# Kernel optimization log

Measured on AMD Instinct MI355X. Metric: run time of the kernel, lower is better.

The kernel has to match this reference:

```python
import math
import numpy as np
import jax
import jax.numpy as jnp
from jax import lax

B, N, F, C, L = 256, 256, 512, 512, 3
RATIO, NEG, BIG_NEG = 0.8, 0.2, -1e9


def setup_inputs():
    key = jax.random.key(0)
    ks = jax.random.split(key, 16)
    g = lambda k, shape, s=0.05: (jax.random.normal(k, shape) * s).astype(jnp.float32)
    x_ids = jax.random.randint(ks[0], (B, N), 0, F)
    graph_prompt_ids = jax.random.randint(ks[1], (B,), 0, F)
    u = jax.random.uniform(ks[2], (B, N, N))
    adj = (u < 16.0 / N).astype(jnp.float32)
    adj = jnp.maximum(adj, jnp.swapaxes(adj, 1, 2))  # undirected
    return dict(
        x_ids=x_ids, graph_prompt_ids=graph_prompt_ids, adj=adj,
        emb=g(ks[3], (F, F), 0.02),
        conv_W=g(ks[4], (L, C, C)), conv_b=jnp.zeros((L, C), jnp.float32),
        att_src=g(ks[5], (L, C)), att_dst=g(ks[6], (L, C)),
        q_W=g(ks[7], (L, C, C)), q_b=jnp.zeros((L, C), jnp.float32),
        att_w=g(ks[8], (L, 2 * C)), att_b=jnp.zeros((L,), jnp.float32),
        gcn_W=g(ks[9], (L, C, C)), gcn_b=jnp.zeros((L, C), jnp.float32),
        le_W1=g(ks[10], (L, C)), le_b1=jnp.zeros((L,), jnp.float32),
        le_W2=g(ks[11], (L, C)), le_W3=g(ks[12], (L, C)),
        lin1_W=g(ks[13], (2 * C, C)), lin1_b=jnp.zeros((C,), jnp.float32),
        lin2_W=g(ks[14], (C, F - 1)), lin2_b=jnp.zeros((F - 1,), jnp.float32),
    )


def _gat(x, mask, W, b, a_src, a_dst):
    # GATConv (heads=1): alpha_ij = softmax_j leaky_relu(a_dst.h_i + a_src.h_j)
    h = x @ W                                   # [B,n,C]
    si = h @ a_dst                              # [B,n] dst term
    sj = h @ a_src                              # [B,n] src term
    logit = jnp.where(mask, jax.nn.leaky_relu(si[:, :, None] + sj[:, None, :], NEG), BIG_NEG)
    att = jax.nn.softmax(logit, axis=-1)
    return jnp.einsum('bij,bjc->bic', att, h) + b


def _gcn(x, A, W, b):
    deg = A.sum(-1)
    d = jnp.where(deg > 0, lax.rsqrt(deg), 0.0)
    return jnp.einsum('bij,bjc->bic', A * d[:, :, None] * d[:, None, :], x @ W) + b


def _neighbor_max(xp, mask):
    # Xq[b,i,c] = max_{j: mask[b,i,j]} xp[b,j,c]; scan over j avoids a [B,n,n,C] tensor
    def step(carry, inp):
        xpj, mj = inp                            # [B,C], [B,n]
        return jnp.maximum(carry, jnp.where(mj[:, :, None], xpj[:, None, :], BIG_NEG)), None
    init = jnp.full(xp.shape, BIG_NEG, xp.dtype)
    Xq, _ = lax.scan(step, init, (jnp.swapaxes(xp, 0, 1), jnp.transpose(mask, (2, 0, 1))))
    return Xq


def _asap_pool(x, A, mask, k, qW, qb, aw, ab, gW, gb, w1, b1, w2, w3):
    c = x.shape[-1]
    xp = _gcn(x, A, gW, gb)                      # intra-cluster GCN
    Xq = _neighbor_max(xp, mask)                 # master query per cluster
    Mq = Xq @ qW + qb
    si = Mq @ aw[:c]
    sj = xp @ aw[c:]
    logit = jnp.where(mask, jax.nn.leaky_relu(si[:, :, None] + sj[:, None, :] + ab, NEG), BIG_NEG)
    S = jax.nn.softmax(logit, axis=-1)           # soft cluster assignment [B,n,n]
    xc = jnp.einsum('bij,bjc->bic', S, x)        # cluster representations
    # LEConv fitness: lin1(x_i) + sum_j A_ij (lin2(x_i) - lin3(x_j)), output dim 1
    deg = A.sum(-1)
    fit = jax.nn.sigmoid(xc @ w1 + b1 + (xc @ w2) * deg - jnp.einsum('bij,bj->bi', A, xc @ w3))
    vals, perm = lax.top_k(fit, k)               # per-graph top-k clusters (static k)
    xk = jnp.take_along_axis(xc, perm[:, :, None], axis=1) * vals[:, :, None]
    Sk = jnp.take_along_axis(S, perm[:, :, None], axis=1)    # [B,k,n]
    SA = jnp.einsum('bkn,bnm->bkm', Sk, A)
    A_new = jnp.einsum('bkm,blm->bkl', SA, Sk)   # S A S^T coarsened adjacency
    diag = jnp.diagonal(A_new, axis1=1, axis2=2)
    A_new = A_new + jnp.eye(k, dtype=A_new.dtype) * jnp.where(diag <= 0, 1.0, 0.0)[:, :, None]
    return xk, A_new, A_new > 0


def _forward(x_ids, adj, emb, conv_W, conv_b, att_src, att_dst, q_W, q_b, att_w, att_b,
             gcn_W, gcn_b, le_W1, le_b1, le_W2, le_W3, lin1_W, lin1_b, lin2_W, lin2_b):
    A = jnp.maximum(adj, jnp.eye(N, dtype=adj.dtype))        # add self loops, weight 1
    mask = A > 0
    x = emb[x_ids]                                           # [B,N,F] embedding lookup
    n, xs = N, None
    for l in range(L):
        k = int(math.ceil(RATIO * n))
        x = jax.nn.relu(_gat(x, mask, conv_W[l], conv_b[l], att_src[l], att_dst[l]))
        x, A, mask = _asap_pool(x, A, mask, k, q_W[l], q_b[l], att_w[l], att_b[l],
                                gcn_W[l], gcn_b[l], le_W1[l], le_b1[l], le_W2[l], le_W3[l])
        r = jnp.concatenate([x.mean(axis=1), x.max(axis=1)], axis=-1)  # scatter mean/max readout
        xs = r if xs is None else xs + r
        n = k
    h = jax.nn.relu(xs @ lin1_W + lin1_b)
    return h @ lin2_W + lin2_b                               # [B, F-1]


def reference(x_ids, graph_prompt_ids, adj, emb, conv_W, conv_b, att_src, att_dst,
              q_W, q_b, att_w, att_b, gcn_W, gcn_b, le_W1, le_b1, le_W2, le_W3,
              lin1_W, lin1_b, lin2_W, lin2_b):
    del graph_prompt_ids  # unused in the original forward body
    return _forward(x_ids, adj, emb, conv_W, conv_b, att_src, att_dst, q_W, q_b,
                    att_w, att_b, gcn_W, gcn_b, le_W1, le_b1, le_W2, le_W3,
                    lin1_W, lin1_b, lin2_W, lin2_b)
```

## Files before the change

kernel.cpp:

```cpp
#include <hip/hip_runtime.h>
#include <math.h>

#define NB   256
#define NMAX 256
#define CH   512
#define LD2  256
#define LDC  512
#define BS2  (256*256)
#define BSC  (256*512)

typedef _Float16 f16;
typedef __attribute__((ext_vector_type(4))) f16 f16x4;
typedef __attribute__((ext_vector_type(8))) f16 f16x8;
typedef __attribute__((ext_vector_type(4))) float f32x4;

#define INV2048 4.8828125e-04f

__device__ __forceinline__ float warp_sum_f(float v) {
#pragma unroll
  for (int m = 32; m >= 1; m >>= 1) v += __shfl_xor(v, m);
  return v;
}

__device__ __forceinline__ void split1(float x, f16& h, f16& l) {
  float xh = (__builtin_fabsf(x) >= 6.103515625e-05f) ? x : 0.f;
  f16 hh = (f16)xh;
  float hf = (float)hh;
  h = hh;
  l = (f16)((x - hf) * 2048.0f);
}

__device__ __forceinline__ float rc(f16 h, f16 l) {
  return (float)h + (float)l * INV2048;
}

__device__ __forceinline__ float rc8q(const f16x8& h, const f16x8& l, int q) {
  return (float)h[q] + (float)l[q] * INV2048;
}

template <int BMODE>
__global__ __launch_bounds__(256, 2)
void pgemm_kernel(const f16* __restrict__ Ahp, const f16* __restrict__ Alp, long bsA, int lda,
                  const f16* __restrict__ Bhp, const f16* __restrict__ Blp, long bsB, int ldb,
                  f16* __restrict__ Yh, f16* __restrict__ Yl, float* __restrict__ Yf,
                  long bsY, int ldy,
                  const float* __restrict__ bias, const float* __restrict__ rowscale,
                  int M, int Ncol, int K, int flags)
{
  __shared__ f16 Ah[64][40];
  __shared__ f16 Al[64][40];
  __shared__ f16 Bh[128][40];
  __shared__ f16 Bl[128][40];

  const int gx = gridDim.x, gy = gridDim.y;
  const int nwg = gx * gy * gridDim.z;
  const int lin = blockIdx.x + gx * (blockIdx.y + gy * blockIdx.z);
  const int q8 = nwg >> 3, r8 = nwg & 7;
  const int xcd = lin & 7, sub = lin >> 3;
  const int swz = ((xcd < r8) ? xcd * (q8 + 1) : r8 * (q8 + 1) + (xcd - r8) * q8) + sub;
  const int bxi = swz % gx;
  const int tmp = swz / gx;
  const int byi = tmp % gy;
  const int b   = tmp / gy;

  const int i0  = byi * 64;
  const int n0  = bxi * 128;
  const int tid = threadIdx.x;
  const int w  = tid >> 6, l = tid & 63;
  const int wr = (w >> 1) * 32, wc = (w & 1) * 64;
  const int lr = l & 15, lq = l >> 4;
  const f16* Abh = Ahp + (long)b * bsA;
  const f16* Abl = Alp + (long)b * bsA;
  const f16* Bbh = Bhp + (long)b * bsB;
  const f16* Bbl = Blp + (long)b * bsB;

  f32x4 acc1[2][4], acc2[2][4];
#pragma unroll
  for (int mi = 0; mi < 2; ++mi)
#pragma unroll
    for (int ni = 0; ni < 4; ++ni) {
      acc1[mi][ni] = (f32x4){0.f, 0.f, 0.f, 0.f};
      acc2[mi][ni] = (f32x4){0.f, 0.f, 0.f, 0.f};
    }

  const f16x8 z8 = (f16x8){0,0,0,0,0,0,0,0};
  f16x8 rah, ral;
  f16x8 rbh[2], rbl[2];
  f16x8 rva, rvb, rwa, rwb;

  const int arow = tid >> 2, akq = (tid & 3) * 8;

  auto LOADA = [&](int k0) {
    int gr = i0 + arow, gk = k0 + akq;
    rah = z8; ral = z8;
    if (gr < M) {
      if (gk + 7 < K) {
        rah = *(const f16x8*)(Abh + (long)gr * lda + gk);
        ral = *(const f16x8*)(Abl + (long)gr * lda + gk);
      } else {
#pragma unroll
        for (int j = 0; j < 8; ++j) if (gk + j < K) {
          rah[j] = Abh[(long)gr * lda + gk + j];
          ral[j] = Abl[(long)gr * lda + gk + j];
        }
      }
    }
  };
  auto STOREA = [&]() {
    *(f16x8*)&Ah[arow][akq] = rah;
    *(f16x8*)&Al[arow][akq] = ral;
  };
  auto LOADB = [&](int k0) {
    if (BMODE == 0) {
#pragma unroll
      for (int rep = 0; rep < 2; ++rep) {
        int idx = rep * 256 + tid;
        int c = idx >> 2, kq = (idx & 3) * 8;
        int gc = n0 + c, gk = k0 + kq;
        rbh[rep] = z8; rbl[rep] = z8;
        if (gc < Ncol) {
          if (gk + 7 < K) {
            rbh[rep] = *(const f16x8*)(Bbh + (long)gc * ldb + gk);
            rbl[rep] = *(const f16x8*)(Bbl + (long)gc * ldb + gk);
          } else {
#pragma unroll
            for (int j = 0; j < 8; ++j) if (gk + j < K) {
              rbh[rep][j] = Bbh[(long)gc * ldb + gk + j];
              rbl[rep][j] = Bbl[(long)gc * ldb + gk + j];
            }
          }
        }
      }
    } else {
      int c8  = (tid >> 4) * 8;
      int k0p = (tid & 15) * 2;
      int gc = n0 + c8;
      rva = z8; rvb = z8; rwa = z8; rwb = z8;
      int gka = k0 + k0p, gkb = gka + 1;
      if (gc + 7 < Ncol) {
        if (gka < K) { rva = *(const f16x8*)(Bbh + (long)gka * ldb + gc);
                       rwa = *(const f16x8*)(Bbl + (long)gka * ldb + gc); }
        if (gkb < K) { rvb = *(const f16x8*)(Bbh + (long)gkb * ldb + gc);
                       rwb = *(const f16x8*)(Bbl + (long)gkb * ldb + gc); }
      }
    }
  };
  auto STOREB = [&]() {
    if (BMODE == 0) {
#pragma unroll
      for (int rep = 0; rep < 2; ++rep) {
        int idx = rep * 256 + tid;
        int c = idx >> 2, kq = (idx & 3) * 8;
        *(f16x8*)&Bh[c][kq] = rbh[rep];
        *(f16x8*)&Bl[c][kq] = rbl[rep];
      }
    } else {
      int c8  = (tid >> 4) * 8;
      int k0p = (tid & 15) * 2;
#pragma unroll
      for (int j = 0; j < 8; ++j) {
        union { f16 f[2]; unsigned u; } ph, pl;
        ph.f[0] = rva[j]; ph.f[1] = rvb[j];
        pl.f[0] = rwa[j]; pl.f[1] = rwb[j];
        *(unsigned*)&Bh[c8 + j][k0p] = ph.u;
        *(unsigned*)&Bl[c8 + j][k0p] = pl.u;
      }
    }
  };

  const int nk = (K + 31) / 32;
  LOADA(0); LOADB(0);
  for (int ki = 0; ki < nk; ++ki) {
    STOREA(); STOREB();
    __syncthreads();
    if (ki + 1 < nk) { LOADA((ki + 1) * 32); LOADB((ki + 1) * 32); }

    f16x8 bh[4], bl[4];
#pragma unroll
    for (int ni = 0; ni < 4; ++ni) {
      bh[ni] = *(const f16x8*)&Bh[wc + ni * 16 + lr][lq * 8];
      bl[ni] = *(const f16x8*)&Bl[wc + ni * 16 + lr][lq * 8];
    }
#pragma unroll
    for (int mi = 0; mi < 2; ++mi) {
      f16x8 ah = *(const f16x8*)&Ah[wr + mi * 16 + lr][lq * 8];
      f16x8 al = *(const f16x8*)&Al[wr + mi * 16 + lr][lq * 8];
#pragma unroll
      for (int ni = 0; ni < 4; ++ni) {
        acc1[mi][ni] = __builtin_amdgcn_mfma_f32_16x16x32_f16(ah, bh[ni], acc1[mi][ni], 0, 0, 0);
        acc2[mi][ni] = __builtin_amdgcn_mfma_f32_16x16x32_f16(ah, bl[ni], acc2[mi][ni], 0, 0, 0);
        acc2[mi][ni] = __builtin_amdgcn_mfma_f32_16x16x32_f16(al, bh[ni], acc2[mi][ni], 0, 0, 0);
      }
    }
    __syncthreads();
  }

#pragma unroll
  for (int mi = 0; mi < 2; ++mi) {
#pragma unroll
    for (int ni = 0; ni < 4; ++ni) {
      int col = n0 + wc + ni * 16 + lr;
      if (col >= Ncol) continue;
      float bv = (flags & 1) ? bias[col] : 0.f;
#pragma unroll
      for (int r = 0; r < 4; ++r) {
        int row = i0 + wr + mi * 16 + lq * 4 + r;
        if (row >= M) continue;
        float vv = acc1[mi][ni][r] + acc2[mi][ni][r] * INV2048;
        if (flags & 4) vv *= rowscale[b * 256 + row];
        vv += bv;
        if (flags & 2) vv = fmaxf(vv, 0.f);
        long off = (long)b * bsY + (long)row * ldy + col;
        if (flags & 8) { f16 h, lo; split1(vv, h, lo); Yh[off] = h; Yl[off] = lo; }
        if (flags & 16) Yf[off] = vv;
      }
    }
  }
}

__global__ void presplit_kernel(const float* __restrict__ W, f16* __restrict__ Wh,
                                f16* __restrict__ Wl, int K, int N) {
  int n = blockIdx.x;
  for (int k = threadIdx.x; k < K; k += blockDim.x) {
    f16 h, l; split1(W[(long)k * N + n], h, l);
    Wh[(long)n * K + k] = h;
    Wl[(long)n * K + k] = l;
  }
}

__global__ void splitbuf_kernel(const float* __restrict__ X, f16* __restrict__ Xh,
                                f16* __restrict__ Xl, int cols) {
  int i = blockIdx.x;
  for (int c = threadIdx.x; c < cols; c += blockDim.x) {
    f16 h, l; split1(X[(long)i * cols + c], h, l);
    Xh[(long)i * cols + c] = h;
    Xl[(long)i * cols + c] = l;
  }
}

__global__ void build_a_deg_kernel(const float* __restrict__ adj, f16* __restrict__ AAh,
                                   f16* __restrict__ AAl, float* __restrict__ deg,
                                   float* __restrict__ dinv) {
  int b = blockIdx.y, i = blockIdx.x, j = threadIdx.x;
  __shared__ float red[256];
  float v = adj[(long)b * BS2 + i * 256 + j];
  if (i == j) v = fmaxf(v, 1.f);
  f16 h, l; split1(v, h, l);
  long o = (long)b * BS2 + i * 256 + j;
  AAh[o] = h; AAl[o] = l;
  red[j] = v; __syncthreads();
  for (int s = 128; s > 0; s >>= 1) { if (j < s) red[j] += red[j + s]; __syncthreads(); }
  if (j == 0) {
    float s = red[0];
    deg[b * 256 + i] = s;
    dinv[b * 256 + i] = (s > 0.f) ? (1.f / sqrtf(s)) : 0.f;
  }
}

__global__ void embed_kernel(const int* __restrict__ ids, const float* __restrict__ emb,
                             f16* __restrict__ Xh, f16* __restrict__ Xl) {
  int b = blockIdx.y, i = blockIdx.x, t = threadIdx.x;
  int id = ids[b * NMAX + i];
  float4 v = *(const float4*)(emb + (long)id * CH + t * 4);
  long o = (long)b * BSC + (long)i * LDC + t * 4;
  float vv[4] = {v.x, v.y, v.z, v.w};
#pragma unroll
  for (int j = 0; j < 4; ++j) { f16 h, l; split1(vv[j], h, l); Xh[o + j] = h; Xl[o + j] = l; }
}

__global__ void rowdot_kernel(const f16* __restrict__ Xh, const f16* __restrict__ Xl,
                              const float* __restrict__ v1, const float* __restrict__ v2,
                              const float* __restrict__ v3,
                              float* __restrict__ o1, float* __restrict__ o2,
                              float* __restrict__ o3, int nvec) {
  int b = blockIdx.y, i = blockIdx.x, lane = threadIdx.x;
  long base = (long)b * BSC + (long)i * LDC;
  float a1 = 0.f, a2 = 0.f, a3 = 0.f;
  for (int c = lane; c < CH; c += 64) {
    float x = rc(Xh[base + c], Xl[base + c]);
    a1 = fmaf(x, v1[c], a1);
    if (nvec > 1) a2 = fmaf(x, v2[c], a2);
    if (nvec > 2) a3 = fmaf(x, v3[c], a3);
  }
  a1 = warp_sum_f(a1);
  if (nvec > 1) a2 = warp_sum_f(a2);
  if (nvec > 2) a3 = warp_sum_f(a3);
  if (lane == 0) {
    o1[b * 256 + i] = a1;
    if (nvec > 1) o2[b * 256 + i] = a2;
    if (nvec > 2) o3[b * 256 + i] = a3;
  }
}

__global__ void vq_kernel(const float* __restrict__ qW, const float* __restrict__ qb,
                          const float* __restrict__ aw, float* __restrict__ v,
                          float* __restrict__ c0) {
  int blk = blockIdx.x, lane = threadIdx.x;
  if (blk < 512) {
    float s = 0.f;
    for (int j = lane; j < CH; j += 64) s = fmaf(qW[(long)blk * CH + j], aw[j], s);
    s = warp_sum_f(s);
    if (lane == 0) v[blk] = s;
  } else {
    float s = 0.f;
    for (int j = lane; j < CH; j += 64) s = fmaf(qb[j], aw[j], s);
    s = warp_sum_f(s);
    if (lane == 0) c0[0] = s;
  }
}

__global__ __launch_bounds__(256)
void softmax_kernel(const f16* __restrict__ AAh, const f16* __restrict__ AAl,
                    const float* __restrict__ si, const float* __restrict__ sj,
                    const float* __restrict__ attb,
                    f16* __restrict__ Ph, f16* __restrict__ Pl, int n, int masked) {
  int b = blockIdx.y, i = blockIdx.x, j = threadIdx.x;
  __shared__ float red[256];
  float logit = -1e30f, e = 0.f;
  float siv = si[b * 256 + i];
  long ro = (long)b * BS2 + i * 256;
  if (j < n) {
    float z = siv + sj[b * 256 + j] + (attb ? attb[0] : 0.f);
    z = (z > 0.f) ? z : 0.2f * z;
    if (masked) {
      float a = rc(AAh[ro + j], AAl[ro + j]);
      logit = (a > 0.f) ? z : -1e9f;
    } else logit = z;
  }
  red[j] = logit; __syncthreads();
  for (int s = 128; s > 0; s >>= 1) { if (j < s) red[j] = fmaxf(red[j], red[j + s]); __syncthreads(); }
  float mx = red[0]; __syncthreads();
  if (j < n) e = expf(logit - mx);
  red[j] = e; __syncthreads();
  for (int s = 128; s > 0; s >>= 1) { if (j < s) red[j] += red[j + s]; __syncthreads(); }
  float sum = red[0];
  if (j < n) {
    f16 h, l; split1(e / sum, h, l);
    Ph[ro + j] = h; Pl[ro + j] = l;
  }
}

__global__ __launch_bounds__(512)
void colmax_kernel(const f16* __restrict__ XPh, const f16* __restrict__ XPl,
                   const float* __restrict__ v, const float* __restrict__ c0,
                   float* __restrict__ si_full, int n) {
  int b = blockIdx.x, t = threadIdx.x;
  int cg = t >> 3, rl = t & 7, c0c = cg * 8;
  long base = (long)b * BSC;
  __shared__ float red[64];
  float m[8];
#pragma unroll
  for (int q = 0; q < 8; ++q) m[q] = -1e9f;
  for (int j = rl; j < n; j += 8) {
    f16x8 h = *(const f16x8*)(XPh + base + (long)j * LDC + c0c);
    f16x8 l = *(const f16x8*)(XPl + base + (long)j * LDC + c0c);
#pragma unroll
    for (int q = 0; q < 8; ++q) m[q] = fmaxf(m[q], rc8q(h, l, q));
  }
#pragma unroll
  for (int d = 1; d < 8; d <<= 1)
#pragma unroll
    for (int q = 0; q < 8; ++q) m[q] = fmaxf(m[q], __shfl_xor(m[q], d));
  if (rl == 0) {
    float p = 0.f;
#pragma unroll
    for (int q = 0; q < 8; ++q) p = fmaf(m[q], v[c0c + q], p);
    red[cg] = p;
  }
  __syncthreads();
  for (int s = 32; s > 0; s >>= 1) { if (t < s) red[t] += red[t + s]; __syncthreads(); }
  if (t == 0) si_full[b] = red[0] + c0[0];
}

__global__ __launch_bounds__(256)
void nbrdot_kernel(const f16* __restrict__ AAh, const f16* __restrict__ AAl,
                   const f16* __restrict__ XPh, const f16* __restrict__ XPl,
                   const float* __restrict__ v, const float* __restrict__ c0,
                   const float* __restrict__ si_full, float* __restrict__ si, int n) {
  int b = blockIdx.y, i = blockIdx.x, t = threadIdx.x;
  __shared__ int list[256];
  __shared__ int cnt, nmiss;
  __shared__ float red[256];
  if (t == 0) { cnt = 0; nmiss = 0; }
  __syncthreads();
  long ro = (long)b * BS2 + i * 256;
  if (t < n) {
    float a = rc(AAh[ro + t], AAl[ro + t]);
    if (a > 0.f) { int p = atomicAdd(&cnt, 1); list[p] = t; }
    else atomicAdd(&nmiss, 1);
  }
  __syncthreads();
  if (nmiss == 0) {
    if (t == 0) si[b * 256 + i] = si_full[b];
    return;
  }
  int c = cnt;
  long base = (long)b * BSC;
  float m1 = -1e9f, m2 = -1e9f;
  for (int q = 0; q < c; ++q) {
    int j = list[q];
    m1 = fmaxf(m1, rc(XPh[base + (long)j * LDC + t], XPl[base + (long)j * LDC + t]));
    m2 = fmaxf(m2, rc(XPh[base + (long)j * LDC + t + 256], XPl[base + (long)j * LDC + t + 256]));
  }
  red[t] = m1 * v[t] + m2 * v[t + 256];
  __syncthreads();
  for (int s = 128; s > 0; s >>= 1) { if (t < s) red[t] += red[t + s]; __syncthreads(); }
  if (t == 0) si[b * 256 + i] = red[0] + c0[0];
}

__global__ void fit_kernel(const f16* __restrict__ AAh, const f16* __restrict__ AAl,
                           const float* __restrict__ t1, const float* __restrict__ t2,
                           const float* __restrict__ t3,
                           const float* __restrict__ deg, const float* __restrict__ leb1,
                           float* __restrict__ fit, int n) {
  int b = blockIdx.y, i = blockIdx.x, lane = threadIdx.x;
  long ro = (long)b * BS2 + i * 256;
  float s = 0.f;
  for (int j = lane; j < n; j += 64) s = fmaf(rc(AAh[ro + j], AAl[ro + j]), t3[b * 256 + j], s);
  s = warp_sum_f(s);
  if (lane == 0) {
    float z = t1[b * 256 + i] + leb1[0] + t2[b * 256 + i] * deg[b * 256 + i] - s;
    fit[b * 256 + i] = 1.f / (1.f + expf(-z));
  }
}

__global__ __launch_bounds__(256)
void topk_kernel(const float* __restrict__ fit, int* __restrict__ perm,
                 float* __restrict__ vals, int n, int k) {
  __shared__ float v[256];
  __shared__ int ix[256];
  int b = blockIdx.x, t = threadIdx.x;
  v[t] = (t < n) ? fit[b * 256 + t] : -1e30f;
  ix[t] = t;
  __syncthreads();
  for (int size = 2; size <= 256; size <<= 1)
    for (int str = size >> 1; str > 0; str >>= 1) {
      int p = t ^ str;
      if (p > t) {
        bool desc = ((t & size) == 0);
        float v1 = v[t], v2 = v[p]; int i1 = ix[t], i2 = ix[p];
        bool inorder = (v1 > v2) || (v1 == v2 && i1 < i2);
        if (inorder != desc) { v[t] = v2; v[p] = v1; ix[t] = i2; ix[p] = i1; }
      }
      __syncthreads();
    }
  if (t < k) { perm[b * 256 + t] = ix[t]; vals[b * 256 + t] = v[t]; }
}

__global__ __launch_bounds__(256)
void gather_kernel(const f16* __restrict__ Hh, const f16* __restrict__ Hl,
                   const f16* __restrict__ Ph, const f16* __restrict__ Pl,
                   const int* __restrict__ perm, const float* __restrict__ vals,
                   f16* __restrict__ Xh, f16* __restrict__ Xl,
                   f16* __restrict__ Skh, f16* __restrict__ Skl, int n) {
  int b = blockIdx.y, p = blockIdx.x, t = threadIdx.x;
  int src = perm[b * 256 + p];
  float sv = vals[b * 256 + p];
#pragma unroll
  for (int r = 0; r < 2; ++r) {
    int c = t + r * 256;
    long so = (long)b * BSC + (long)src * LDC + c;
    long dof = (long)b * BSC + (long)p * LDC + c;
    float x = rc(Hh[so], Hl[so]) * sv;
    f16 h, l; split1(x, h, l);
    Xh[dof] = h; Xl[dof] = l;
  }
  if (t < n) {
    long so = (long)b * BS2 + src * 256 + t;
    long dof = (long)b * BSC + p * 256 + t;
    Skh[dof] = Ph[so]; Skl[dof] = Pl[so];
  }
}

__global__ void degfix_kernel(f16* __restrict__ AAh, f16* __restrict__ AAl,
                              float* __restrict__ deg, float* __restrict__ dinv, int k) {
  int b = blockIdx.y, i = blockIdx.x, j = threadIdx.x;
  __shared__ float red[256];
  long ro = (long)b * BS2 + i * 256;
  float v = 0.f;
  if (j < k) {
    v = rc(AAh[ro + j], AAl[ro + j]);
    if (j == i && v <= 0.f) {
      v += 1.f;
      f16 h, l; split1(v, h, l);
      AAh[ro + j] = h; AAl[ro + j] = l;
    }
  }
  red[j] = v; __syncthreads();
  for (int s = 128; s > 0; s >>= 1) { if (j < s) red[j] += red[j + s]; __syncthreads(); }
  if (j == 0) {
// ... 240 lines not shown
                  const float* __restrict__ w3, const float* __restrict__ leb1,
                  float* __restrict__ xs, int n) {
  int b = blockIdx.x, t = threadIdx.x;
  int cg = t >> 3, rl = t & 7, c0c = cg * 8;
  long baseC = (long)b * BSC;
  __shared__ float red[512];
  __shared__ float xc2[512];

  float s8[8];
#pragma unroll
  for (int q = 0; q < 8; ++q) s8[q] = 0.f;
  for (int j = rl; j < n; j += 8) {
    f16x8 h = *(const f16x8*)(Xh + baseC + (long)j * LDC + c0c);
    f16x8 l = *(const f16x8*)(Xl + baseC + (long)j * LDC + c0c);
#pragma unroll
    for (int q = 0; q < 8; ++q) s8[q] += rc8q(h, l, q);
  }
#pragma unroll
  for (int d = 1; d < 8; d <<= 1)
#pragma unroll
    for (int q = 0; q < 8; ++q) s8[q] += __shfl_xor(s8[q], d);
  float invn = 1.f / (float)n;
  if (rl == 0) {
#pragma unroll
    for (int q = 0; q < 8; ++q) xc2[c0c + q] = s8[q] * invn;
  }
  __syncthreads();

  float x2 = xc2[t];
  red[t] = x2 * w1[t]; __syncthreads();
  for (int s2 = 256; s2 > 0; s2 >>= 1) { if (t < s2) red[t] += red[t + s2]; __syncthreads(); }
  float a1 = red[0]; __syncthreads();
  red[t] = x2 * w2[t]; __syncthreads();
  for (int s2 = 256; s2 > 0; s2 >>= 1) { if (t < s2) red[t] += red[t + s2]; __syncthreads(); }
  float a2 = red[0]; __syncthreads();
  red[t] = x2 * w3[t]; __syncthreads();
  for (int s2 = 256; s2 > 0; s2 >>= 1) { if (t < s2) red[t] += red[t + s2]; __syncthreads(); }
  float a3 = red[0]; __syncthreads();

  float alpha = sc[b * 16 + 2], deg3 = sc[b * 16 + 3];
  float sub = 0.f;
  for (int j = 0; j < n; ++j) sub += alpha * a3;
  float z = a1 + leb1[0] + a2 * deg3 - sub;
  float fv = 1.f / (1.f + expf(-z));
  xs[b * 1024 + t] += fv * x2;
  xs[b * 1024 + 512 + t] += fv * x2;
  (void)Hh; (void)Hl; (void)gb;
}

extern "C" void kernel_launch(void* const* d_in, const int* in_sizes, int n_in,
                              void* d_out, int out_size, void* d_ws, size_t ws_size,
                              hipStream_t stream) {
  (void)in_sizes; (void)n_in; (void)out_size;
  const int*   x_ids  = (const int*)  d_in[0];
  const float* adj    = (const float*)d_in[2];
  const float* emb    = (const float*)d_in[3];
  const float* conv_W = (const float*)d_in[4];
  const float* conv_b = (const float*)d_in[5];
  const float* att_src= (const float*)d_in[6];
  const float* att_dst= (const float*)d_in[7];
  const float* q_W    = (const float*)d_in[8];
  const float* q_b    = (const float*)d_in[9];
  const float* att_w  = (const float*)d_in[10];
  const float* att_b  = (const float*)d_in[11];
  const float* gcn_W  = (const float*)d_in[12];
  const float* gcn_b  = (const float*)d_in[13];
  const float* le_W1  = (const float*)d_in[14];
  const float* le_b1  = (const float*)d_in[15];
  const float* le_W2  = (const float*)d_in[16];
  const float* le_W3  = (const float*)d_in[17];
  const float* lin1_W = (const float*)d_in[18];
  const float* lin1_b = (const float*)d_in[19];
  const float* lin2_W = (const float*)d_in[20];
  const float* lin2_b = (const float*)d_in[21];
  float* out = (float*)d_out;

  const size_t WN_CONV = 3u * CH * CH;
  const size_t WN_GCN  = 3u * CH * CH;
  const size_t WN_L1   = (size_t)(2 * CH) * CH;
  const size_t WN_L2   = (size_t)CH * 511;
  const size_t WTOT    = WN_CONV + WN_GCN + WN_L1 + WN_L2;

  const size_t per_b  = (size_t)(3 * BSC * 4 + 2 * BS2 * 4 + 11 * 256 * 4
                                 + (4 * 512 + 2 * 256 + 16) * 4 + 4096);
  const size_t fixedb = (size_t)(3 * 512 + 64 + NB * 1024 + NB * 512) * 4
                      + WTOT * 4 + (size_t)NB * 1024 * 4 + (size_t)NB * 512 * 4;
  const size_t slack  = 64 * 512;
  int bc = 4;
  for (int cand = 256; cand >= 4; cand >>= 1) {
    if ((size_t)cand * per_b + fixedb + slack <= ws_size) { bc = cand; break; }
  }
  const int nchunks = NB / bc;

  char* w = (char*)d_ws;
  auto alloc = [&](size_t bytes) { char* p = w; w += (bytes + 255) & ~(size_t)255; return p; };
  float* xs   = (float*)alloc(sizeof(float) * NB * 1024);
  float* vvec = (float*)alloc(sizeof(float) * 3 * CH);
  float* c0   = (float*)alloc(256);
  f16*   Wh   = (f16*)alloc(WTOT * 2);
  f16*   Wl   = (f16*)alloc(WTOT * 2);
  f16*   XSh  = (f16*)alloc((size_t)NB * 1024 * 2);
  f16*   XSl  = (f16*)alloc((size_t)NB * 1024 * 2);
  f16*   FHh  = (f16*)alloc((size_t)NB * 512 * 2);
  f16*   FHl  = (f16*)alloc((size_t)NB * 512 * 2);
  f16* Xh  = (f16*)alloc((size_t)bc * BSC * 2);
  f16* Xl  = (f16*)alloc((size_t)bc * BSC * 2);
  f16* Hh  = (f16*)alloc((size_t)bc * BSC * 2);
  f16* Hl  = (f16*)alloc((size_t)bc * BSC * 2);
  f16* XPh = (f16*)alloc((size_t)bc * BSC * 2);
  f16* XPl = (f16*)alloc((size_t)bc * BSC * 2);
  f16* Ph  = (f16*)alloc((size_t)bc * BS2 * 2);
  f16* Pl  = (f16*)alloc((size_t)bc * BS2 * 2);
  f16* AAh = (f16*)alloc((size_t)bc * BS2 * 2);
  f16* AAl = (f16*)alloc((size_t)bc * BS2 * 2);
  float* si   = (float*)alloc(sizeof(float) * bc * NMAX);
  float* sj   = (float*)alloc(sizeof(float) * bc * NMAX);
  float* deg  = (float*)alloc(sizeof(float) * bc * NMAX);
  float* dinv = (float*)alloc(sizeof(float) * bc * NMAX);
  float* t1   = (float*)alloc(sizeof(float) * bc * NMAX);
  float* t2   = (float*)alloc(sizeof(float) * bc * NMAX);
  float* t3   = (float*)alloc(sizeof(float) * bc * NMAX);
  float* fit  = (float*)alloc(sizeof(float) * bc * NMAX);
  float* vals = (float*)alloc(sizeof(float) * bc * NMAX);
  int*   perm = (int*)  alloc(sizeof(int)   * bc * NMAX);
  float* sifu = (float*)alloc(sizeof(float) * bc);
  float* wv   = (float*)alloc(sizeof(float) * bc * 256);
  float* xcr  = (float*)alloc(sizeof(float) * bc * 512);
  float* h3   = (float*)alloc(sizeof(float) * bc * 512);
  float* sc   = (float*)alloc(sizeof(float) * bc * 16);
  f16* xcrh   = (f16*)alloc((size_t)bc * 512 * 2);
  f16* xcrl   = (f16*)alloc((size_t)bc * 512 * 2);

  f16* cwh = Wh;                       f16* cwl = Wl;
  f16* gwh = Wh + WN_CONV;             f16* gwl = Wl + WN_CONV;
  f16* l1h = Wh + WN_CONV + WN_GCN;    f16* l1l = Wl + WN_CONV + WN_GCN;
  f16* l2h = l1h + WN_L1;              f16* l2l = l1l + WN_L1;

  hipMemsetAsync(xs, 0, sizeof(float) * NB * 1024, stream);

  for (int l = 0; l < 3; ++l) {
    presplit_kernel<<<512, 256, 0, stream>>>(conv_W + (size_t)l * CH * CH,
                                             cwh + (size_t)l * CH * CH,
                                             cwl + (size_t)l * CH * CH, CH, CH);
    presplit_kernel<<<512, 256, 0, stream>>>(gcn_W + (size_t)l * CH * CH,
                                             gwh + (size_t)l * CH * CH,
                                             gwl + (size_t)l * CH * CH, CH, CH);
    vq_kernel<<<513, 64, 0, stream>>>(q_W + (size_t)l * CH * CH, q_b + l * CH,
                                      att_w + (size_t)l * 2 * CH, vvec + l * CH, c0 + l);
  }
  presplit_kernel<<<512, 256, 0, stream>>>(lin1_W, l1h, l1l, 2 * CH, CH);
  presplit_kernel<<<511, 256, 0, stream>>>(lin2_W, l2h, l2l, CH, 511);

  for (int ch = 0; ch < nchunks; ++ch) {
    const int b0 = ch * bc;
    const int*   ids_c = x_ids + (size_t)b0 * NMAX;
    const float* adj_c = adj + (size_t)b0 * BS2;
    float*       xs_c  = xs + (size_t)b0 * 1024;

    build_a_deg_kernel<<<dim3(NMAX, bc), 256, 0, stream>>>(adj_c, AAh, AAl, deg, dinv);
    embed_kernel<<<dim3(NMAX, bc), 128, 0, stream>>>(ids_c, emb, Xh, Xl);

    {
      const int n = 256, kk = 205;
      const float* aw = att_w;
      pgemm_kernel<0><<<dim3(4, 4, bc), 256, 0, stream>>>(
          Xh, Xl, BSC, LDC, cwh, cwl, 0, CH,
          Hh, Hl, nullptr, BSC, LDC, nullptr, nullptr, n, CH, CH, 8);
      rowdot_kernel<<<dim3(n, bc), 64, 0, stream>>>(Hh, Hl, att_dst, att_src, nullptr,
                                                    si, sj, nullptr, 2);
      softmax_kernel<<<dim3(n, bc), 256, 0, stream>>>(AAh, AAl, si, sj, nullptr, Ph, Pl, n, 1);
      pgemm_kernel<1><<<dim3(4, 4, bc), 256, 0, stream>>>(
          Ph, Pl, BS2, LD2, Hh, Hl, BSC, LDC,
          Xh, Xl, nullptr, BSC, LDC, conv_b, nullptr, n, CH, n, 1 | 2 | 8);
      pgemm_kernel<0><<<dim3(4, 4, bc), 256, 0, stream>>>(
          Xh, Xl, BSC, LDC, gwh, gwl, 0, CH,
          Hh, Hl, nullptr, BSC, LDC, nullptr, dinv, n, CH, CH, 4 | 8);
      pgemm_kernel<1><<<dim3(4, 4, bc), 256, 0, stream>>>(
          AAh, AAl, BS2, LD2, Hh, Hl, BSC, LDC,
          XPh, XPl, nullptr, BSC, LDC, gcn_b, dinv, n, CH, n, 1 | 4 | 8);
      rowdot_kernel<<<dim3(n, bc), 64, 0, stream>>>(XPh, XPl, aw + CH, nullptr, nullptr,
                                                    sj, nullptr, nullptr, 1);
      colmax_kernel<<<bc, 512, 0, stream>>>(XPh, XPl, vvec, c0, sifu, n);
      nbrdot_kernel<<<dim3(n, bc), 256, 0, stream>>>(AAh, AAl, XPh, XPl, vvec, c0, sifu, si, n);
      softmax_kernel<<<dim3(n, bc), 256, 0, stream>>>(AAh, AAl, si, sj, att_b, Ph, Pl, n, 1);
      pgemm_kernel<1><<<dim3(4, 4, bc), 256, 0, stream>>>(
          Ph, Pl, BS2, LD2, Xh, Xl, BSC, LDC,
          Hh, Hl, nullptr, BSC, LDC, nullptr, nullptr, n, CH, n, 8);
      rowdot_kernel<<<dim3(n, bc), 64, 0, stream>>>(Hh, Hl, le_W1, le_W2, le_W3,
                                                    t1, t2, t3, 3);
      fit_kernel<<<dim3(n, bc), 64, 0, stream>>>(AAh, AAl, t1, t2, t3, deg, le_b1, fit, n);
      topk_kernel<<<bc, 256, 0, stream>>>(fit, perm, vals, n, kk);
      gather_kernel<<<dim3(kk, bc), 256, 0, stream>>>(Hh, Hl, Ph, Pl, perm, vals,
                                                      Xh, Xl, XPh, XPl, n);
      pgemm_kernel<0><<<dim3(2, 4, bc), 256, 0, stream>>>(
          XPh, XPl, BSC, LD2, AAh, AAl, BS2, LD2,
          Ph, Pl, nullptr, BS2, LD2, nullptr, nullptr, kk, n, n, 8);
      pgemm_kernel<0><<<dim3(2, 4, bc), 256, 0, stream>>>(
          Ph, Pl, BS2, LD2, XPh, XPl, BSC, LD2,
          AAh, AAl, nullptr, BS2, LD2, nullptr, nullptr, kk, kk, n, 8);
      degfix_kernel<<<dim3(kk, bc), 256, 0, stream>>>(AAh, AAl, deg, dinv, kk);
      readout_kernel<<<dim3(2, bc), 256, 0, stream>>>(Xh, Xl, xs_c, kk);
    }

    {
      const int n = 205, kk = 164;
      const float* aw = att_w + (size_t)2 * CH;
      pgemm_kernel<0><<<dim3(4, 4, bc), 256, 0, stream>>>(
          Xh, Xl, BSC, LDC, cwh + (size_t)CH * CH, cwl + (size_t)CH * CH, 0, CH,
          Hh, Hl, nullptr, BSC, LDC, nullptr, nullptr, n, CH, CH, 8);
      rowdot_kernel<<<dim3(n, bc), 64, 0, stream>>>(Hh, Hl, att_dst + CH, att_src + CH, nullptr,
                                                    si, sj, nullptr, 2);
      softmax_kernel<<<dim3(n, bc), 256, 0, stream>>>(AAh, AAl, si, sj, nullptr, Ph, Pl, n, 0);
      pgemm_kernel<1><<<dim3(4, 4, bc), 256, 0, stream>>>(
          Ph, Pl, BS2, LD2, Hh, Hl, BSC, LDC,
          Xh, Xl, nullptr, BSC, LDC, conv_b + CH, nullptr, n, CH, n, 1 | 2 | 8);
      pgemm_kernel<0><<<dim3(4, 4, bc), 256, 0, stream>>>(
          Xh, Xl, BSC, LDC, gwh + (size_t)CH * CH, gwl + (size_t)CH * CH, 0, CH,
          Hh, Hl, nullptr, BSC, LDC, nullptr, dinv, n, CH, CH, 4 | 8);
      pgemm_kernel<1><<<dim3(4, 4, bc), 256, 0, stream>>>(
          AAh, AAl, BS2, LD2, Hh, Hl, BSC, LDC,
          XPh, XPl, nullptr, BSC, LDC, gcn_b + CH, dinv, n, CH, n, 1 | 4 | 8);
      rowdot_kernel<<<dim3(n, bc), 64, 0, stream>>>(XPh, XPl, aw + CH, nullptr, nullptr,
                                                    sj, nullptr, nullptr, 1);
      pool2_kernel<<<bc, 512, 0, stream>>>(
          XPh, XPl, Xh, Xl, AAh, AAl, sj, vvec + CH, c0 + 1, att_b + 1,
          le_W1 + CH, le_W2 + CH, le_W3 + CH, xcr, xcrh, xcrl, t1, t2, t3, sc, n, kk);
      fit_kernel<<<dim3(n, bc), 64, 0, stream>>>(AAh, AAl, t1, t2, t3, deg, le_b1 + 1, fit, n);
      topk_kernel<<<bc, 256, 0, stream>>>(fit, perm, vals, n, kk);
      readout_rank1_kernel<<<bc, 256, 0, stream>>>(vals, xcr, xs_c, kk);
    }

    {
      const int n = 164;
      pgemm_kernel<0><<<dim3(4, 1, 1), 256, 0, stream>>>(
          xcrh, xcrl, 0, 512, cwh + (size_t)2 * CH * CH, cwl + (size_t)2 * CH * CH, 0, CH,
          nullptr, nullptr, h3, 0, 512, nullptr, nullptr, bc, CH, CH, 16);
      gat3scal_kernel<<<bc, 64, 0, stream>>>(h3, att_dst + 2 * CH, att_src + 2 * CH, sc);
      gatw_kernel<<<dim3(n, bc), 256, 0, stream>>>(vals, sc, wv, n);
      xgat_kernel<<<dim3(n, bc), 256, 0, stream>>>(wv, h3, conv_b + 2 * CH, Xh, Xl);
      pool3_kernel<<<bc, 512, 0, stream>>>(
          Hh, Hl, Xh, Xl, sc, gcn_b + 2 * CH,
          le_W1 + 2 * CH, le_W2 + 2 * CH, le_W3 + 2 * CH, le_b1 + 2, xs_c, n);
    }
  }

  splitbuf_kernel<<<NB, 256, 0, stream>>>(xs, XSh, XSl, 1024);
  pgemm_kernel<0><<<dim3(4, 4, 1), 256, 0, stream>>>(
      XSh, XSl, 0, 1024, l1h, l1l, 0, 1024,
      FHh, FHl, nullptr, 0, CH, lin1_b, nullptr, NB, CH, 2 * CH, 1 | 2 | 8);
  pgemm_kernel<0><<<dim3(4, 4, 1), 256, 0, stream>>>(
      FHh, FHl, 0, CH, l2h, l2l, 0, CH,
      nullptr, nullptr, out, 0, 511, lin2_b, nullptr, NB, 511, CH, 1 | 16);
}
```

Baseline: 3.415 ms.

## Shrink GEMM tile to 64x64 and replace colmax/nbrdot with split-channel neighbor max

```diff
diff --git a/kernel.cpp b/kernel.cpp
--- a/kernel.cpp
+++ b/kernel.cpp
@@ -49,8 +49,8 @@
 {
   __shared__ f16 Ah[64][40];
   __shared__ f16 Al[64][40];
-  __shared__ f16 Bh[128][40];
-  __shared__ f16 Bl[128][40];
+  __shared__ f16 Bh[64][40];
+  __shared__ f16 Bl[64][40];
 
   const int gx = gridDim.x, gy = gridDim.y;
   const int nwg = gx * gy * gridDim.z;
@@ -64,28 +64,28 @@
   const int b   = tmp / gy;
 
   const int i0  = byi * 64;
-  const int n0  = bxi * 128;
+  const int n0  = bxi * 64;
   const int tid = threadIdx.x;
   const int w  = tid >> 6, l = tid & 63;
-  const int wr = (w >> 1) * 32, wc = (w & 1) * 64;
+  const int wr = (w >> 1) * 32, wc = (w & 1) * 32;
   const int lr = l & 15, lq = l >> 4;
   const f16* Abh = Ahp + (long)b * bsA;
   const f16* Abl = Alp + (long)b * bsA;
   const f16* Bbh = Bhp + (long)b * bsB;
   const f16* Bbl = Blp + (long)b * bsB;
 
-  f32x4 acc1[2][4], acc2[2][4];
+  f32x4 acc1[2][2], acc2[2][2];
 #pragma unroll
   for (int mi = 0; mi < 2; ++mi)
 #pragma unroll
-    for (int ni = 0; ni < 4; ++ni) {
+    for (int ni = 0; ni < 2; ++ni) {
       acc1[mi][ni] = (f32x4){0.f, 0.f, 0.f, 0.f};
       acc2[mi][ni] = (f32x4){0.f, 0.f, 0.f, 0.f};
     }
 
   const f16x8 z8 = (f16x8){0,0,0,0,0,0,0,0};
   f16x8 rah, ral;
-  f16x8 rbh[2], rbl[2];
+  f16x8 rbh, rbl;
   f16x8 rva, rvb, rwa, rwb;
 
   const int arow = tid >> 2, akq = (tid & 3) * 8;
@@ -112,58 +112,52 @@
   };
   auto LOADB = [&](int k0) {
     if (BMODE == 0) {
-#pragma unroll
-      for (int rep = 0; rep < 2; ++rep) {
-        int idx = rep * 256 + tid;
-        int c = idx >> 2, kq = (idx & 3) * 8;
-        int gc = n0 + c, gk = k0 + kq;
-        rbh[rep] = z8; rbl[rep] = z8;
-        if (gc < Ncol) {
-          if (gk + 7 < K) {
-            rbh[rep] = *(const f16x8*)(Bbh + (long)gc * ldb + gk);
-            rbl[rep] = *(const f16x8*)(Bbl + (long)gc * ldb + gk);
-          } else {
-#pragma unroll
-            for (int j = 0; j < 8; ++j) if (gk + j < K) {
-              rbh[rep][j] = Bbh[(long)gc * ldb + gk + j];
-              rbl[rep][j] = Bbl[(long)gc * ldb + gk + j];
-            }
+      int gc = n0 + arow, gk = k0 + akq;
+      rbh = z8; rbl = z8;
+      if (gc < Ncol) {
+        if (gk + 7 < K) {
+          rbh = *(const f16x8*)(Bbh + (long)gc * ldb + gk);
+          rbl = *(const f16x8*)(Bbl + (long)gc * ldb + gk);
+        } else {
+#pragma unroll
+          for (int j = 0; j < 8; ++j) if (gk + j < K) {
+            rbh[j] = Bbh[(long)gc * ldb + gk + j];
+            rbl[j] = Bbl[(long)gc * ldb + gk + j];
           }
         }
       }
     } else {
-      int c8  = (tid >> 4) * 8;
-      int k0p = (tid & 15) * 2;
-      int gc = n0 + c8;
-      rva = z8; rvb = z8; rwa = z8; rwb = z8;
-      int gka = k0 + k0p, gkb = gka + 1;
-      if (gc + 7 < Ncol) {
-        if (gka < K) { rva = *(const f16x8*)(Bbh + (long)gka * ldb + gc);
-                       rwa = *(const f16x8*)(Bbl + (long)gka * ldb + gc); }
-        if (gkb < K) { rvb = *(const f16x8*)(Bbh + (long)gkb * ldb + gc);
-                       rwb = *(const f16x8*)(Bbl + (long)gkb * ldb + gc); }
+      if (tid < 128) {
+        int c8  = (tid >> 4) * 8;
+        int k0p = (tid & 15) * 2;
+        int gc = n0 + c8;
+        rva = z8; rvb = z8; rwa = z8; rwb = z8;
+        int gka = k0 + k0p, gkb = gka + 1;
+        if (gc + 7 < Ncol) {
+          if (gka < K) { rva = *(const f16x8*)(Bbh + (long)gka * ldb + gc);
+                         rwa = *(const f16x8*)(Bbl + (long)gka * ldb + gc); }
+          if (gkb < K) { rvb = *(const f16x8*)(Bbh + (long)gkb * ldb + gc);
+                         rwb = *(const f16x8*)(Bbl + (long)gkb * ldb + gc); }
+        }
       }
     }
   };
   auto STOREB = [&]() {
     if (BMODE == 0) {
-#pragma unroll
-      for (int rep = 0; rep < 2; ++rep) {
-        int idx = rep * 256 + tid;
-        int c = idx >> 2, kq = (idx & 3) * 8;
-        *(f16x8*)&Bh[c][kq] = rbh[rep];
-        *(f16x8*)&Bl[c][kq] = rbl[rep];
-      }
+      *(f16x8*)&Bh[arow][akq] = rbh;
+      *(f16x8*)&Bl[arow][akq] = rbl;
     } else {
-      int c8  = (tid >> 4) * 8;
-      int k0p = (tid & 15) * 2;
-#pragma unroll
-      for (int j = 0; j < 8; ++j) {
-        union { f16 f[2]; unsigned u; } ph, pl;
-        ph.f[0] = rva[j]; ph.f[1] = rvb[j];
-        pl.f[0] = rwa[j]; pl.f[1] = rwb[j];
-        *(unsigned*)&Bh[c8 + j][k0p] = ph.u;
-        *(unsigned*)&Bl[c8 + j][k0p] = pl.u;
+      if (tid < 128) {
+        int c8  = (tid >> 4) * 8;
+        int k0p = (tid & 15) * 2;
+#pragma unroll
+        for (int j = 0; j < 8; ++j) {
+          union { f16 f[2]; unsigned u; } ph, pl;
+          ph.f[0] = rva[j]; ph.f[1] = rvb[j];
+          pl.f[0] = rwa[j]; pl.f[1] = rwb[j];
+          *(unsigned*)&Bh[c8 + j][k0p] = ph.u;
+          *(unsigned*)&Bl[c8 + j][k0p] = pl.u;
+        }
       }
     }
   };
@@ -175,9 +169,9 @@
     __syncthreads();
     if (ki + 1 < nk) { LOADA((ki + 1) * 32); LOADB((ki + 1) * 32); }
 
-    f16x8 bh[4], bl[4];
-#pragma unroll
-    for (int ni = 0; ni < 4; ++ni) {
+    f16x8 bh[2], bl[2];
+#pragma unroll
+    for (int ni = 0; ni < 2; ++ni) {
       bh[ni] = *(const f16x8*)&Bh[wc + ni * 16 + lr][lq * 8];
       bl[ni] = *(const f16x8*)&Bl[wc + ni * 16 + lr][lq * 8];
     }
@@ -186,7 +180,7 @@
       f16x8 ah = *(const f16x8*)&Ah[wr + mi * 16 + lr][lq * 8];
       f16x8 al = *(const f16x8*)&Al[wr + mi * 16 + lr][lq * 8];
 #pragma unroll
-      for (int ni = 0; ni < 4; ++ni) {
+      for (int ni = 0; ni < 2; ++ni) {
         acc1[mi][ni] = __builtin_amdgcn_mfma_f32_16x16x32_f16(ah, bh[ni], acc1[mi][ni], 0, 0, 0);
         acc2[mi][ni] = __builtin_amdgcn_mfma_f32_16x16x32_f16(ah, bl[ni], acc2[mi][ni], 0, 0, 0);
         acc2[mi][ni] = __builtin_amdgcn_mfma_f32_16x16x32_f16(al, bh[ni], acc2[mi][ni], 0, 0, 0);
@@ -198,7 +192,7 @@
 #pragma unroll
   for (int mi = 0; mi < 2; ++mi) {
 #pragma unroll
-    for (int ni = 0; ni < 4; ++ni) {
+    for (int ni = 0; ni < 2; ++ni) {
       int col = n0 + wc + ni * 16 + lr;
       if (col >= Ncol) continue;
       float bv = (flags & 1) ? bias[col] : 0.f;
@@ -272,7 +266,8 @@
                               const float* __restrict__ v1, const float* __restrict__ v2,
                               const float* __restrict__ v3,
                               float* __restrict__ o1, float* __restrict__ o2,
-                              float* __restrict__ o3, int nvec) {
+                              float* __restrict__ o3,
+                              const float* __restrict__ cadd, int nvec) {
   int b = blockIdx.y, i = blockIdx.x, lane = threadIdx.x;
   long base = (long)b * BSC + (long)i * LDC;
   float a1 = 0.f, a2 = 0.f, a3 = 0.f;
@@ -286,7 +281,7 @@
   if (nvec > 1) a2 = warp_sum_f(a2);
   if (nvec > 2) a3 = warp_sum_f(a3);
   if (lane == 0) {
-    o1[b * 256 + i] = a1;
+    o1[b * 256 + i] = a1 + (cadd ? cadd[0] : 0.f);
     if (nvec > 1) o2[b * 256 + i] = a2;
     if (nvec > 2) o3[b * 256 + i] = a3;
   }
@@ -313,11 +308,13 @@
 void softmax_kernel(const f16* __restrict__ AAh, const f16* __restrict__ AAl,
                     const float* __restrict__ si, const float* __restrict__ sj,
                     const float* __restrict__ attb,
-                    f16* __restrict__ Ph, f16* __restrict__ Pl, int n, int masked) {
+                    f16* __restrict__ Ph, f16* __restrict__ Pl, int n, int masked,
+                    int nparts, int pstride) {
   int b = blockIdx.y, i = blockIdx.x, j = threadIdx.x;
   __shared__ float red[256];
   float logit = -1e30f, e = 0.f;
-  float siv = si[b * 256 + i];
+  float siv = 0.f;
+  for (int p = 0; p < nparts; ++p) siv += si[(long)p * pstride + b * 256 + i];
   long ro = (long)b * BS2 + i * 256;
   if (j < n) {
     float z = siv + sj[b * 256 + j] + (attb ? attb[0] : 0.f);
@@ -340,72 +337,57 @@
   }
 }
 
-__global__ __launch_bounds__(512)
-void colmax_kernel(const f16* __restrict__ XPh, const f16* __restrict__ XPl,
-                   const float* __restrict__ v, const float* __restrict__ c0,
-                   float* __restrict__ si_full, int n) {
-  int b = blockIdx.x, t = threadIdx.x;
-  int cg = t >> 3, rl = t & 7, c0c = cg * 8;
-  long base = (long)b * BSC;
-  __shared__ float red[64];
-  float m[8];
-#pragma unroll
-  for (int q = 0; q < 8; ++q) m[q] = -1e9f;
-  for (int j = rl; j < n; j += 8) {
-    f16x8 h = *(const f16x8*)(XPh + base + (long)j * LDC + c0c);
-    f16x8 l = *(const f16x8*)(XPl + base + (long)j * LDC + c0c);
-#pragma unroll
-    for (int q = 0; q < 8; ++q) m[q] = fmaxf(m[q], rc8q(h, l, q));
-  }
-#pragma unroll
-  for (int d = 1; d < 8; d <<= 1)
-#pragma unroll
-    for (int q = 0; q < 8; ++q) m[q] = fmaxf(m[q], __shfl_xor(m[q], d));
-  if (rl == 0) {
-    float p = 0.f;
-#pragma unroll
-    for (int q = 0; q < 8; ++q) p = fmaf(m[q], v[c0c + q], p);
-    red[cg] = p;
-  }
+__global__ __launch_bounds__(256)
+void nbr2_kernel(const f16* __restrict__ AAh, const f16* __restrict__ AAl,
+                 const f16* __restrict__ XPh, const f16* __restrict__ XPl,
+                 const float* __restrict__ v, float* __restrict__ part,
+                 int n, int pstride) {
+  __shared__ f16 Xs_h[256][64];
+  __shared__ f16 Xs_l[256][64];
+  __shared__ float vs[64];
+  const int s = blockIdx.x, b = blockIdx.y, t = threadIdx.x;
+  const int w = t >> 6, lane = t & 63;
+  const int c0c = s * 64;
+  const long baseC = (long)b * BSC;
+  const f16x8 z8 = (f16x8){0,0,0,0,0,0,0,0};
+#pragma unroll
+  for (int rep = 0; rep < 8; ++rep) {
+    int idx = rep * 256 + t;
+    int row = idx >> 3, cq = (idx & 7) * 8;
+    f16x8 h = z8, l = z8;
+    if (row < n) {
+      h = *(const f16x8*)(XPh + baseC + (long)row * LDC + c0c + cq);
+      l = *(const f16x8*)(XPl + baseC + (long)row * LDC + c0c + cq);
+    }
+    *(f16x8*)&Xs_h[row][cq] = h;
+    *(f16x8*)&Xs_l[row][cq] = l;
+  }
+  if (t < 64) vs[t] = v[c0c + t];
   __syncthreads();
-  for (int s = 32; s > 0; s >>= 1) { if (t < s) red[t] += red[t + s]; __syncthreads(); }
-  if (t == 0) si_full[b] = red[0] + c0[0];
-}
-
-__global__ __launch_bounds__(256)
-void nbrdot_kernel(const f16* __restrict__ AAh, const f16* __restrict__ AAl,
-                   const f16* __restrict__ XPh, const f16* __restrict__ XPl,
-                   const float* __restrict__ v, const float* __restrict__ c0,
-                   const float* __restrict__ si_full, float* __restrict__ si, int n) {
-  int b = blockIdx.y, i = blockIdx.x, t = threadIdx.x;
-  __shared__ int list[256];
-  __shared__ int cnt, nmiss;
-  __shared__ float red[256];
-  if (t == 0) { cnt = 0; nmiss = 0; }
-  __syncthreads();
-  long ro = (long)b * BS2 + i * 256;
-  if (t < n) {
-    float a = rc(AAh[ro + t], AAl[ro + t]);
-    if (a > 0.f) { int p = atomicAdd(&cnt, 1); list[p] = t; }
-    else atomicAdd(&nmiss, 1);
-  }
-  __syncthreads();
-  if (nmiss == 0) {
-    if (t == 0) si[b * 256 + i] = si_full[b];
-    return;
-  }
-  int c = cnt;
-  long base = (long)b * BSC;
-  float m1 = -1e9f, m2 = -1e9f;
-  for (int q = 0; q < c; ++q) {
-    int j = list[q];
-    m1 = fmaxf(m1, rc(XPh[base + (long)j * LDC + t], XPl[base + (long)j * LDC + t]));
-    m2 = fmaxf(m2, rc(XPh[base + (long)j * LDC + t + 256], XPl[base + (long)j * LDC + t + 256]));
-  }
-  red[t] = m1 * v[t] + m2 * v[t + 256];
-  __syncthreads();
-  for (int s = 128; s > 0; s >>= 1) { if (t < s) red[t] += red[t + s]; __syncthreads(); }
-  if (t == 0) si[b * 256 + i] = red[0] + c0[0];
+
+  const long ro0 = (long)b * BS2;
+  for (int i = w; i < n; i += 4) {
+    long ro = ro0 + (long)i * 256;
+    unsigned long long mk[4];
+#pragma unroll
+    for (int g = 0; g < 4; ++g) {
+      int j0 = g * 64 + lane;
+      bool nb = (j0 < n) && (rc(AAh[ro + j0], AAl[ro + j0]) > 0.f);
+      mk[g] = __ballot(nb);
+    }
+    float mcol = -1e9f;
+#pragma unroll
+    for (int g = 0; g < 4; ++g) {
+      unsigned long long m_ = mk[g];
+      while (m_) {
+        int j = g * 64 + __builtin_ctzll(m_);
+        m_ &= m_ - 1;
+        mcol = fmaxf(mcol, rc(Xs_h[j][lane], Xs_l[j][lane]));
+      }
+    }
+    float p = warp_sum_f(mcol * vs[lane]);
+    if (lane == 0) part[(long)s * pstride + b * 256 + i] = p;
+  }
 }
 
 __global__ void fit_kernel(const f16* __restrict__ AAh, const f16* __restrict__ AAl,
@@ -812,7 +794,7 @@
   const size_t WTOT    = WN_CONV + WN_GCN + WN_L1 + WN_L2;
 
   const size_t per_b  = (size_t)(3 * BSC * 4 + 2 * BS2 * 4 + 11 * 256 * 4
-                                 + (4 * 512 + 2 * 256 + 16) * 4 + 4096);
+                                 + (4 * 512 + 2 * 256 + 16 + 8 * 256) * 4 + 4096);
   const size_t fixedb = (size_t)(3 * 512 + 64 + NB * 1024 + NB * 512) * 4
                       + WTOT * 4 + (size_t)NB * 1024 * 4 + (size_t)NB * 512 * 4;
   const size_t slack  = 64 * 512;
@@ -853,13 +835,14 @@
   float* fit  = (float*)alloc(sizeof(float) * bc * NMAX);
   float* vals = (float*)alloc(sizeof(float) * bc * NMAX);
   int*   perm = (int*)  alloc(sizeof(int)   * bc * NMAX);
-  float* sifu = (float*)alloc(sizeof(float) * bc);
+  float* part = (float*)alloc(sizeof(float) * 8 * bc * NMAX);
   float* wv   = (float*)alloc(sizeof(float) * bc * 256);
   float* xcr  = (float*)alloc(sizeof(float) * bc * 512);
   float* h3   = (float*)alloc(sizeof(float) * bc * 512);
   float* sc   = (float*)alloc(sizeof(float) * bc * 16);
   f16* xcrh   = (f16*)alloc((size_t)bc * 512 * 2);
   f16* xcrl   = (f16*)alloc((size_t)bc * 512 * 2);
+  (void)si;
 
   f16* cwh = Wh;                       f16* cwl = Wl;
   f16* gwh = Wh + WN_CONV;             f16* gwl = Wl + WN_CONV;
@@ -893,39 +876,41 @@
     {
       const int n = 256, kk = 205;
       const float* aw = att_w;
-      pgemm_kernel<0><<<dim3(4, 4, bc), 256, 0, stream>>>(
+      pgemm_kernel<0><<<dim3(8, 4, bc), 256, 0, stream>>>(
           Xh, Xl, BSC, LDC, cwh, cwl, 0, CH,
           Hh, Hl, nullptr, BSC, LDC, nullptr, nullptr, n, CH, CH, 8);
       rowdot_kernel<<<dim3(n, bc), 64, 0, stream>>>(Hh, Hl, att_dst, att_src, nullptr,
-                                                    si, sj, nullptr, 2);
-      softmax_kernel<<<dim3(n, bc), 256, 0, stream>>>(AAh, AAl, si, sj, nullptr, Ph, Pl, n, 1);
-      pgemm_kernel<1><<<dim3(4, 4, bc), 256, 0, stream>>>(
+                                                    sj, si, nullptr, nullptr, 2);
+      softmax_kernel<<<dim3(n, bc), 256, 0, stream>>>(AAh, AAl, sj, si, nullptr,
+                                                      Ph, Pl, n, 1, 1, 0);
+      pgemm_kernel<1><<<dim3(8, 4, bc), 256, 0, stream>>>(
           Ph, Pl, BS2, LD2, Hh, Hl, BSC, LDC,
           Xh, Xl, nullptr, BSC, LDC, conv_b, nullptr, n, CH, n, 1 | 2 | 8);
-      pgemm_kernel<0><<<dim3(4, 4, bc), 256, 0, stream>>>(
+      pgemm_kernel<0><<<dim3(8, 4, bc), 256, 0, stream>>>(
           Xh, Xl, BSC, LDC, gwh, gwl, 0, CH,
           Hh, Hl, nullptr, BSC, LDC, nullptr, dinv, n, CH, CH, 4 | 8);
-      pgemm_kernel<1><<<dim3(4, 4, bc), 256, 0, stream>>>(
+      pgemm_kernel<1><<<dim3(8, 4, bc), 256, 0, stream>>>(
           AAh, AAl, BS2, LD2, Hh, Hl, BSC, LDC,
           XPh, XPl, nullptr, BSC, LDC, gcn_b, dinv, n, CH, n, 1 | 4 | 8);
       rowdot_kernel<<<dim3(n, bc), 64, 0, stream>>>(XPh, XPl, aw + CH, nullptr, nullptr,
-                                                    sj, nullptr, nullptr, 1);
-      colmax_kernel<<<bc, 512, 0, stream>>>(XPh, XPl, vvec, c0, sifu, n);
-      nbrdot_kernel<<<dim3(n, bc), 256, 0, stream>>>(AAh, AAl, XPh, XPl, vvec, c0, sifu, si, n);
-      softmax_kernel<<<dim3(n, bc), 256, 0, stream>>>(AAh, AAl, si, sj, att_b, Ph, Pl, n, 1);
-      pgemm_kernel<1><<<dim3(4, 4, bc), 256, 0, stream>>>(
+                                                    sj, nullptr, nullptr, c0, 1);
+      nbr2_kernel<<<dim3(8, bc), 256, 0, stream>>>(AAh, AAl, XPh, XPl, vvec, part,
+                                                   n, bc * NMAX);
+      softmax_kernel<<<dim3(n, bc), 256, 0, stream>>>(AAh, AAl, part, sj, att_b,
+                                                      Ph, Pl, n, 1, 8, bc * NMAX);
+      pgemm_kernel<1><<<dim3(8, 4, bc), 256, 0, stream>>>(
           Ph, Pl, BS2, LD2, Xh, Xl, BSC, LDC,
           Hh, Hl, nullptr, BSC, LDC, nullptr, nullptr, n, CH, n, 8);
       rowdot_kernel<<<dim3(n, bc), 64, 0, stream>>>(Hh, Hl, le_W1, le_W2, le_W3,
-                                                    t1, t2, t3, 3);
+                                                    t1, t2, t3, nullptr, 3);
       fit_kernel<<<dim3(n, bc), 64, 0, stream>>>(AAh, AAl, t1, t2, t3, deg, le_b1, fit, n);
       topk_kernel<<<bc, 256, 0, stream>>>(fit, perm, vals, n, kk);
       gather_kernel<<<dim3(kk, bc), 256, 0, stream>>>(Hh, Hl, Ph, Pl, perm, vals,
                                                       Xh, Xl, XPh, XPl, n);
-      pgemm_kernel<0><<<dim3(2, 4, bc), 256, 0, stream>>>(
+      pgemm_kernel<0><<<dim3(4, 4, bc), 256, 0, stream>>>(
           XPh, XPl, BSC, LD2, AAh, AAl, BS2, LD2,
           Ph, Pl, nullptr, BS2, LD2, nullptr, nullptr, kk, n, n, 8);
-      pgemm_kernel<0><<<dim3(2, 4, bc), 256, 0, stream>>>(
+      pgemm_kernel<0><<<dim3(4, 4, bc), 256, 0, stream>>>(
           Ph, Pl, BS2, LD2, XPh, XPl, BSC, LD2,
           AAh, AAl, nullptr, BS2, LD2, nullptr, nullptr, kk, kk, n, 8);
       degfix_kernel<<<dim3(kk, bc), 256, 0, stream>>>(AAh, AAl, deg, dinv, kk);
@@ -935,23 +920,24 @@
     {
       const int n = 205, kk = 164;
       const float* aw = att_w + (size_t)2 * CH;
-      pgemm_kernel<0><<<dim3(4, 4, bc), 256, 0, stream>>>(
+      pgemm_kernel<0><<<dim3(8, 4, bc), 256, 0, stream>>>(
           Xh, Xl, BSC, LDC, cwh + (size_t)CH * CH, cwl + (size_t)CH * CH, 0, CH,
           Hh, Hl, nullptr, BSC, LDC, nullptr, nullptr, n, CH, CH, 8);
       rowdot_kernel<<<dim3(n, bc), 64, 0, stream>>>(Hh, Hl, att_dst + CH, att_src + CH, nullptr,
-                                                    si, sj, nullptr, 2);
-      softmax_kernel<<<dim3(n, bc), 256, 0, stream>>>(AAh, AAl, si, sj, nullptr, Ph, Pl, n, 0);
-      pgemm_kernel<1><<<dim3(4, 4, bc), 256, 0, stream>>>(
+                                                    sj, si, nullptr, nullptr, 2);
+      softmax_kernel<<<dim3(n, bc), 256, 0, stream>>>(AAh, AAl, sj, si, nullptr,
+                                                      Ph, Pl, n, 0, 1, 0);
+      pgemm_kernel<1><<<dim3(8, 4, bc), 256, 0, stream>>>(
           Ph, Pl, BS2, LD2, Hh, Hl, BSC, LDC,
           Xh, Xl, nullptr, BSC, LDC, conv_b + CH, nullptr, n, CH, n, 1 | 2 | 8);
-      pgemm_kernel<0><<<dim3(4, 4, bc), 256, 0, stream>>>(
+      pgemm_kernel<0><<<dim3(8, 4, bc), 256, 0, stream>>>(
           Xh, Xl, BSC, LDC, gwh + (size_t)CH * CH, gwl + (size_t)CH * CH, 0, CH,
           Hh, Hl, nullptr, BSC, LDC, nullptr, dinv, n, CH, CH, 4 | 8);
-      pgemm_kernel<1><<<dim3(4, 4, bc), 256, 0, stream>>>(
+      pgemm_kernel<1><<<dim3(8, 4, bc), 256, 0, stream>>>(
           AAh, AAl, BS2, LD2, Hh, Hl, BSC, LDC,
           XPh, XPl, nullptr, BSC, LDC, gcn_b + CH, dinv, n, CH, n, 1 | 4 | 8);
       rowdot_kernel<<<dim3(n, bc), 64, 0, stream>>>(XPh, XPl, aw + CH, nullptr, nullptr,
-                                                    sj, nullptr, nullptr, 1);
+                                                    sj, nullptr, nullptr, nullptr, 1);
       pool2_kernel<<<bc, 512, 0, stream>>>(
           XPh, XPl, Xh, Xl, AAh, AAl, sj, vvec + CH, c0 + 1, att_b + 1,
           le_W1 + CH, le_W2 + CH, le_W3 + CH, xcr, xcrh, xcrl, t1, t2, t3, sc, n, kk);
@@ -962,7 +948,7 @@
 
     {
       const int n = 164;
-      pgemm_kernel<0><<<dim3(4, 1, 1), 256, 0, stream>>>(
+      pgemm_kernel<0><<<dim3(8, 1, 1), 256, 0, stream>>>(
           xcrh, xcrl, 0, 512, cwh + (size_t)2 * CH * CH, cwl + (size_t)2 * CH * CH, 0, CH,
           nullptr, nullptr, h3, 0, 512, nullptr, nullptr, bc, CH, CH, 16);
       gat3scal_kernel<<<bc, 64, 0, stream>>>(h3, att_dst + 2 * CH, att_src + 2 * CH, sc);
@@ -975,10 +961,10 @@
   }
 
   splitbuf_kernel<<<NB, 256, 0, stream>>>(xs, XSh, XSl, 1024);
-  pgemm_kernel<0><<<dim3(4, 4, 1), 256, 0, stream>>>(
+  pgemm_kernel<0><<<dim3(8, 4, 1), 256, 0, stream>>>(
       XSh, XSl, 0, 1024, l1h, l1l, 0, 1024,
       FHh, FHl, nullptr, 0, CH, lin1_b, nullptr, NB, CH, 2 * CH, 1 | 2 | 8);
-  pgemm_kernel<0><<<dim3(4, 4, 1), 256, 0, stream>>>(
+  pgemm_kernel<0><<<dim3(8, 4, 1), 256, 0, stream>>>(
       FHh, FHl, 0, CH, l2h, l2l, 0, CH,
       nullptr, nullptr, out, 0, 511, lin2_b, nullptr, NB, 511, CH, 1 | 16);
 }
```

Result: slower. 3.737 ms (+9.4%).
